# Kernel optimization log

Measured on AMD Instinct MI355X. Metric: run time of the kernel, lower is better.

The kernel has to match this reference:

```python
import jax, jax.numpy as jnp
import numpy as np

B, N, CQ, H, CH = 1, 256, 128, 4, 32  # batch, n_res, c_q(=c_k=c_v), heads, per-head dim


def setup_inputs() -> dict:
    key = jax.random.key(0)
    ks = jax.random.split(key, 12)
    s = 0.02
    q_x = jax.random.normal(ks[0], (B, N, N, CQ), jnp.float32)
    kv_x = jax.random.normal(ks[1], (B, N, N, CQ), jnp.float32)
    # mask bias: 0 where kept, -1e9 where masked (additive mask)
    keep = jax.random.uniform(ks[2], (B, N, 1, 1, N)) < 0.9
    mask_bias = jnp.where(keep, 0.0, -1e9).astype(jnp.float32)
    triangle_bias = jax.random.normal(ks[3], (B, 1, H, N, N), jnp.float32)
    # projection weights, stored per-head as [H, CH, C_in]
    wq = jax.random.normal(ks[4], (H, CH, CQ), jnp.float32) * s
    wk = jax.random.normal(ks[5], (H, CH, CQ), jnp.float32) * s
    wv = jax.random.normal(ks[6], (H, CH, CQ), jnp.float32) * s
    wg = jax.random.normal(ks[7], (H, CH, CQ), jnp.float32) * s
    bg = jax.random.normal(ks[8], (H, CH), jnp.float32) * s + 1.0  # gating bias init 1
    wo = jax.random.normal(ks[9], (CQ, H * CH), jnp.float32) * s
    bo = jnp.zeros((CQ,), jnp.float32)
    return {"q_x": q_x, "kv_x": kv_x, "mask_bias": mask_bias,
            "triangle_bias": triangle_bias, "wq": wq, "wk": wk, "wv": wv,
            "wg": wg, "bg": bg, "wo": wo, "bo": bo}


def reference(q_x, kv_x, mask_bias, triangle_bias, wq, wk, wv, wg, bg, wo, bo):
    scale = 1.0 / np.sqrt(CH).astype(np.float32)
    # project + split heads: [B,N,Q,C] x [H,D,C] -> [B,N,H,Q,D]
    q = jnp.einsum('bnqc,hdc->bnhqd', q_x, wq) * scale
    k = jnp.einsum('bnkc,hdc->bnhkd', kv_x, wk)
    v = jnp.einsum('bnkc,hdc->bnhkd', kv_x, wv)
    # scores + additive biases (mask_bias broadcasts over h,q; triangle over n)
    a = jnp.einsum('bnhqd,bnhkd->bnhqk', q, k) + mask_bias + triangle_bias
    a = jax.nn.softmax(a, axis=-1)
    o = jnp.einsum('bnhqk,bnhkd->bnhqd', a, v)
    o = jnp.swapaxes(o, -2, -3)  # [B,N,Q,H,D]
    # gating
    g = jax.nn.sigmoid(jnp.einsum('bnqc,hdc->bnqhd', q_x, wg) + bg)
    o = o * g
    o = o.reshape(o.shape[:-2] + (H * CH,))  # [B,N,Q,H*D]
    return jnp.einsum('bnqe,ce->bnqc', o, wo) + bo
```

## Files before the change

### kernel.cpp

```cpp
#include <hip/hip_runtime.h>

#define NRES 256
#define CIN  128
#define NH   4
#define DH   32

typedef __attribute__((ext_vector_type(4))) float f32x4;
typedef __attribute__((ext_vector_type(8))) short bf16x8;
typedef unsigned short u16;

#define U_WQG 0
#define U_WKV 32768
#define U_WWO 65536
#define U_QB  131072
#define U_KB  (U_QB + 8388608)
#define U_VT  (U_KB + 8388608)
#define U_GB  (U_VT + 8388608)
#define WS_NEED ((size_t)(U_GB + 8388608) * 2)

__device__ __forceinline__ unsigned pkbf(float a, float b) {
    unsigned ua = __builtin_bit_cast(unsigned, a);
    unsigned ub = __builtin_bit_cast(unsigned, b);
    ua += 0x7fffu + ((ua >> 16) & 1u);
    ub += 0x7fffu + ((ub >> 16) & 1u);
    return __builtin_amdgcn_perm(ub, ua, 0x07060302);
}
__device__ __forceinline__ u16 f2bfu(float f) {
    unsigned u = __builtin_bit_cast(unsigned, f);
    return (u16)((u + 0x7fffu + ((u >> 16) & 1u)) >> 16);
}
__device__ __forceinline__ float bf2f(u16 v) {
    unsigned u = ((unsigned)v) << 16;
    return __builtin_bit_cast(float, u);
}
union bfr { unsigned u[4]; bf16x8 v; };
__device__ __forceinline__ bf16x8 ldcvt8(const float* __restrict__ p) {
    f32x4 a = *(const f32x4*)p; f32x4 b = *(const f32x4*)(p + 4);
    bfr r;
    r.u[0] = pkbf(a[0], a[1]); r.u[1] = pkbf(a[2], a[3]);
    r.u[2] = pkbf(b[0], b[1]); r.u[3] = pkbf(b[2], b[3]);
    return r.v;
}
__device__ __forceinline__ bf16x8 ldcvt8s(const float* __restrict__ p, float sc) {
    f32x4 a = *(const f32x4*)p; f32x4 b = *(const f32x4*)(p + 4);
    bfr r;
    r.u[0] = pkbf(a[0] * sc, a[1] * sc); r.u[1] = pkbf(a[2] * sc, a[3] * sc);
    r.u[2] = pkbf(b[0] * sc, b[1] * sc); r.u[3] = pkbf(b[2] * sc, b[3] * sc);
    return r.v;
}
__device__ __forceinline__ void stage16(const float* __restrict__ p, u16* dst) {
    f32x4 a = *(const f32x4*)p,     b = *(const f32x4*)(p + 4);
    f32x4 c = *(const f32x4*)(p + 8), d = *(const f32x4*)(p + 12);
    bfr x, y;
    x.u[0] = pkbf(a[0], a[1]); x.u[1] = pkbf(a[2], a[3]);
    x.u[2] = pkbf(b[0], b[1]); x.u[3] = pkbf(b[2], b[3]);
    y.u[0] = pkbf(c[0], c[1]); y.u[1] = pkbf(c[2], c[3]);
    y.u[2] = pkbf(d[0], d[1]); y.u[3] = pkbf(d[2], d[3]);
    *(bf16x8*)dst = x.v;
    *(bf16x8*)(dst + 8) = y.v;
}
#define MFMA(a, b, c) __builtin_amdgcn_mfma_f32_16x16x32_bf16((a), (b), (c), 0, 0, 0)

__global__ void wconv(const float* __restrict__ wq, const float* __restrict__ wk,
                      const float* __restrict__ wv, const float* __restrict__ wg,
                      const float* __restrict__ wo, u16* __restrict__ ws)
{
    const int i0 = (blockIdx.x * 256 + threadIdx.x) * 8;
    const float qsc = 0.17677669529663687f;
    const float* src; u16* dst; float sc = 1.f;
    if (i0 < 32768) {
        const int e = i0 >> 7, c = i0 & 127;
        src = (e < 128 ? wq + e * CIN : wg + (e - 128) * CIN) + c;
        if (e < 128) sc = qsc;
        dst = ws + U_WQG + i0;
    } else if (i0 < 65536) {
        const int j = i0 - 32768, e = j >> 7, c = j & 127;
        src = (e < 128 ? wk + e * CIN : wv + (e - 128) * CIN) + c;
        dst = ws + U_WKV + j;
    } else {
        const int j = i0 - 65536;
        src = wo + j; dst = ws + U_WWO + j;
    }
    *(bf16x8*)dst = ldcvt8s(src, sc);
}

#define XST 136
__global__ __launch_bounds__(256, 4) void proj(
    const float* __restrict__ q_x, const float* __restrict__ kv_x,
    const float* __restrict__ bg, u16* __restrict__ ws)
{
    const int t = threadIdx.x, lane = t & 63, w = t >> 6;
    const int mrow = lane & 15, grp = lane >> 4;
    const int koff = grp * 8, rbase = grp * 4;
    const int R0 = blockIdx.x * 32;
    const int ysel = blockIdx.y;
    const float* __restrict__ src = ysel ? kv_x : q_x;
    const u16* __restrict__ W = ws + (ysel ? U_WKV : U_WQG);

    __shared__ u16 Xs[32 * XST];

    {
        const int row = t >> 3, c0 = (t & 7) * 16;
        stage16(src + (size_t)(R0 + row) * CIN + c0, &Xs[row * XST + c0]);
    }
    __syncthreads();

    const int cb = w * 64;
    const u16* __restrict__ Wc = W + (size_t)cb * CIN;

    const f32x4 zf = {0.f, 0.f, 0.f, 0.f};
    f32x4 acc[2][4];
    #pragma unroll
    for (int rt = 0; rt < 2; ++rt)
        #pragma unroll
        for (int nt = 0; nt < 4; ++nt) acc[rt][nt] = zf;

    #pragma unroll
    for (int ct = 0; ct < 4; ++ct) {
        const int c0 = ct * 32 + koff;
        bf16x8 a0 = *(const bf16x8*)&Xs[mrow * XST + c0];
        bf16x8 a1 = *(const bf16x8*)&Xs[(16 + mrow) * XST + c0];
        #pragma unroll
        for (int nt = 0; nt < 4; ++nt) {
            bf16x8 bw = *(const bf16x8*)(Wc + (size_t)(nt * 16 + mrow) * CIN + c0);
            acc[0][nt] = MFMA(a0, bw, acc[0][nt]);
            acc[1][nt] = MFMA(a1, bw, acc[1][nt]);
        }
    }

    if (!ysel) {
        if (cb < 128) {
            #pragma unroll
            for (int nt = 0; nt < 4; ++nt) {
                const int e = cb + nt * 16 + mrow;
                #pragma unroll
                for (int rt = 0; rt < 2; ++rt)
                    #pragma unroll
                    for (int r = 0; r < 4; ++r)
                        ws[U_QB + (size_t)(R0 + rt * 16 + rbase + r) * CIN + e] =
                            f2bfu(acc[rt][nt][r]);
            }
        } else {
            #pragma unroll
            for (int nt = 0; nt < 4; ++nt) {
                const int e = cb - 128 + nt * 16 + mrow;
                const float b = bg[e];
                #pragma unroll
                for (int rt = 0; rt < 2; ++rt)
                    #pragma unroll
                    for (int r = 0; r < 4; ++r) {
                        const float g = 1.f / (1.f + __expf(-(acc[rt][nt][r] + b)));
                        ws[U_GB + (size_t)(R0 + rt * 16 + rbase + r) * CIN + e] = f2bfu(g);
                    }
            }
        }
    } else {
        if (cb < 128) {
            #pragma unroll
            for (int nt = 0; nt < 4; ++nt) {
                const int e = cb + nt * 16 + mrow;
                #pragma unroll
                for (int rt = 0; rt < 2; ++rt)
                    #pragma unroll
                    for (int r = 0; r < 4; ++r)
                        ws[U_KB + (size_t)(R0 + rt * 16 + rbase + r) * CIN + e] =
                            f2bfu(acc[rt][nt][r]);
            }
        } else {
            const int n = R0 >> 8;
            #pragma unroll
            for (int nt = 0; nt < 4; ++nt) {
                const int d = cb - 128 + nt * 16 + mrow;
                #pragma unroll
                for (int rt = 0; rt < 2; ++rt) {
                    const int k0 = (R0 & 255) + rt * 16 + rbase;
                    uint2 v;
                    v.x = pkbf(acc[rt][nt][0], acc[rt][nt][1]);
                    v.y = pkbf(acc[rt][nt][2], acc[rt][nt][3]);
                    *(uint2*)&ws[U_VT + ((size_t)n * 128 + d) * 256 + k0] = v;
                }
            }
        }
    }
}

#define PST 40
__global__ __launch_bounds__(256, 4) void flash(
    const u16* __restrict__ ws, const float* __restrict__ mask_bias,
    const float* __restrict__ tri_bias, float* __restrict__ o_out)
{
    const int h = blockIdx.x, n = blockIdx.y;
    const int t = threadIdx.x, lane = t & 63, w = t >> 6;
    const int mrow = lane & 15, grp = lane >> 4;
    const int koff = grp * 8, rbase = grp * 4;
    const int q0 = w * 64;

    __shared__ u16 Pt[4 * 64 * PST];
    __shared__ float msk[NRES];

    if (t < 64) *(float4*)&msk[t * 4] = *(const float4*)(mask_bias + n * NRES + t * 4);

    const u16* __restrict__ Qb = ws + U_QB + (size_t)n * NRES * CIN;
    const u16* __restrict__ Kb = ws + U_KB + (size_t)n * NRES * CIN;
    const u16* __restrict__ Vt = ws + U_VT + (size_t)n * 128 * 256;
    const u16* __restrict__ Gb = ws + U_GB + (size_t)n * NRES * CIN;
    const float* __restrict__ trih = tri_bias + (size_t)h * NRES * NRES;

    bf16x8 bq[4];
    #pragma unroll
    for (int qt = 0; qt < 4; ++qt)
        bq[qt] = *(const bf16x8*)(Qb + (size_t)(q0 + qt * 16 + mrow) * CIN + h * DH + koff);
    __syncthreads();

    const f32x4 zf = {0.f, 0.f, 0.f, 0.f};
    f32x4 oa[4][2];
    float ls[4] = {0.f, 0.f, 0.f, 0.f};
    #pragma unroll
    for (int qt = 0; qt < 4; ++qt) { oa[qt][0] = zf; oa[qt][1] = zf; }

    u16* __restrict__ pw = &Pt[w * 64 * PST];

    for (int kt = 0; kt < 8; ++kt) {
        const int kb = kt * 32;
        bf16x8 ak0 = *(const bf16x8*)(Kb + (size_t)(kb + mrow) * CIN + h * DH + koff);
        bf16x8 ak1 = *(const bf16x8*)(Kb + (size_t)(kb + 16 + mrow) * CIN + h * DH + koff);
        bf16x8 bv0 = *(const bf16x8*)(Vt + (size_t)(h * DH + mrow) * NRES + kb + koff);
        bf16x8 bv1 = *(const bf16x8*)(Vt + (size_t)(h * DH + 16 + mrow) * NRES + kb + koff);
        f32x4 mk0 = *(const f32x4*)&msk[kb + rbase];
        f32x4 mk1 = *(const f32x4*)&msk[kb + 16 + rbase];
        #pragma unroll
        for (int r = 0; r < 4; ++r) { mk0[r] -= 8.f; mk1[r] -= 8.f; }

        #pragma unroll
        for (int qt = 0; qt < 4; ++qt) {
            f32x4 s0 = MFMA(ak0, bq[qt], zf);
            f32x4 s1 = MFMA(ak1, bq[qt], zf);
            const float* __restrict__ tq =
                trih + (size_t)(q0 + qt * 16 + mrow) * NRES + kb + rbase;
            f32x4 t0 = *(const f32x4*)tq;
            f32x4 t1 = *(const f32x4*)(tq + 16);
            #pragma unroll
            for (int r = 0; r < 4; ++r) {
                s0[r] = __expf(s0[r] + t0[r] + mk0[r]);
                s1[r] = __expf(s1[r] + t1[r] + mk1[r]);
            }
            ls[qt] += s0[0] + s0[1] + s0[2] + s0[3] + s1[0] + s1[1] + s1[2] + s1[3];
            uint2 p0, p1;
            p0.x = pkbf(s0[0], s0[1]); p0.y = pkbf(s0[2], s0[3]);
            p1.x = pkbf(s1[0], s1[1]); p1.y = pkbf(s1[2], s1[3]);
            *(uint2*)&pw[(qt * 16 + mrow) * PST + rbase] = p0;
            *(uint2*)&pw[(qt * 16 + mrow) * PST + 16 + rbase] = p1;
        }
        asm volatile("s_waitcnt lgkmcnt(0)" ::: "memory");
        #pragma unroll
        for (int qt = 0; qt < 4; ++qt) {
            bf16x8 pa = *(const bf16x8*)&pw[(qt * 16 + mrow) * PST + koff];
            oa[qt][0] = MFMA(pa, bv0, oa[qt][0]);
            oa[qt][1] = MFMA(pa, bv1, oa[qt][1]);
        }
    }

    float* __restrict__ orow = o_out + (size_t)n * NRES * CIN + h * DH;
    #pragma unroll
    for (int qt = 0; qt < 4; ++qt) {
        float lred = ls[qt];
        lred += __shfl_xor(lred, 16, 64);
        lred += __shfl_xor(lred, 32, 64);
        const float linv = 1.f / lred;
        #pragma unroll
        for (int r = 0; r < 4; ++r) {
            const float iv = __shfl(linv, rbase + r, 64);
            const int q = q0 + qt * 16 + rbase + r;
            const float g0 = bf2f(Gb[(size_t)q * CIN + h * DH + mrow]);
            const float g1 = bf2f(Gb[(size_t)q * CIN + h * DH + 16 + mrow]);
            orow[q * CIN + mrow]      = oa[qt][0][r] * iv * g0;
            orow[q * CIN + 16 + mrow] = oa[qt][1][r] * iv * g1;
        }
    }
}

__global__ __launch_bounds__(256, 4) void gout(
    const u16* __restrict__ ws, const float* __restrict__ bo, float* io)
{
    const int t = threadIdx.x, lane = t & 63, w = t >> 6;
    const int mrow = lane & 15, grp = lane >> 4;
    const int koff = grp * 8, rbase = grp * 4;
    const int r0 = blockIdx.x * 64;
    const u16* __restrict__ Wo = ws + U_WWO;

    __shared__ u16 Xs[64 * XST];

    {
        const int row = t >> 2, c0 = (t & 3) * 32;
        const float* p = io + (size_t)(r0 + row) * CIN + c0;
        stage16(p,      &Xs[row * XST + c0]);
        stage16(p + 16, &Xs[row * XST + c0 + 16]);
    }
    __syncthreads();

    const int rw = w * 16;
    const f32x4 zf = {0.f, 0.f, 0.f, 0.f};
    f32x4 acc[8];
    #pragma unroll
    for (int nt = 0; nt < 8; ++nt) acc[nt] = zf;

    #pragma unroll
    for (int ct = 0; ct < 4; ++ct) {
        const int c0 = ct * 32 + koff;
        bf16x8 a0 = *(const bf16x8*)&Xs[(rw + mrow) * XST + c0];
        #pragma unroll
        for (int nt = 0; nt < 8; ++nt) {
            bf16x8 bw = *(const bf16x8*)(Wo + (size_t)(nt * 16 + mrow) * CIN + c0);
            acc[nt] = MFMA(a0, bw, acc[nt]);
        }
    }

    #pragma unroll
    for (int nt = 0; nt < 8; ++nt) {
        const float bc = bo[nt * 16 + mrow];
        #pragma unroll
        for (int r = 0; r < 4; ++r)
            io[(size_t)(r0 + rw + rbase + r) * CIN + nt * 16 + mrow] = acc[nt][r] + bc;
    }
}

#define KST 32
#define VST 264
#define GST 136

__global__ __launch_bounds__(256, 3) void attn_fb(
    const float* __restrict__ q_x, const float* __restrict__ kv_x,
    const float* __restrict__ mask_bias, const float* __restrict__ tri_bias,
    const float* __restrict__ wq, const float* __restrict__ wk,
    const float* __restrict__ wv, float* __restrict__ o_out)
{
    const int h = blockIdx.x, n = blockIdx.y;
    const int t = threadIdx.x;
    const int lane = t & 63, w = t >> 6;
    const int mrow = lane & 15;
    const int grp  = lane >> 4;
    const int koff = grp * 8;
    const int rbase = grp * 4;
    const int q0 = w * 64;

    __shared__ u16 Ks[NRES * KST];
    __shared__ u16 Vt[DH * VST];
    __shared__ u16 Ptb[4 * 32 * PST];
    __shared__ float msk[NRES];

    if (t < 64) *(float4*)&msk[t * 4] = *(const float4*)(mask_bias + n * NRES + t * 4);

    const float* __restrict__ qxn = q_x  + (size_t)n * NRES * CIN;
    const float* __restrict__ kxn = kv_x + (size_t)n * NRES * CIN;
    const float* __restrict__ wqh = wq + h * DH * CIN;
    const float* __restrict__ wkh = wk + h * DH * CIN;
    const float* __restrict__ wvh = wv + h * DH * CIN;

    f32x4 aq_[4][2], ak_[4][2], av_[4][2];
    const f32x4 zf = {0.f, 0.f, 0.f, 0.f};
    #pragma unroll
    for (int qt = 0; qt < 4; ++qt)
        #pragma unroll
        for (int dt = 0; dt < 2; ++dt) { aq_[qt][dt] = zf; ak_[qt][dt] = zf; av_[qt][dt] = zf; }

    const float qsc = 0.17677669529663687f;
    #pragma unroll
    for (int ct = 0; ct < 4; ++ct) {
        const int c0 = ct * 32 + koff;
        bf16x8 bq0 = ldcvt8s(wqh + mrow * CIN + c0, qsc);
        bf16x8 bq1 = ldcvt8s(wqh + (16 + mrow) * CIN + c0, qsc);
        bf16x8 bk0 = ldcvt8(wkh + mrow * CIN + c0);
        bf16x8 bk1 = ldcvt8(wkh + (16 + mrow) * CIN + c0);
        bf16x8 bv0 = ldcvt8(wvh + mrow * CIN + c0);
        bf16x8 bv1 = ldcvt8(wvh + (16 + mrow) * CIN + c0);
        #pragma unroll
        for (int qt = 0; qt < 4; ++qt) {
            bf16x8 aX = ldcvt8(qxn + (q0 + qt * 16 + mrow) * CIN + c0);
            aq_[qt][0] = MFMA(aX, bq0, aq_[qt][0]);
            aq_[qt][1] = MFMA(aX, bq1, aq_[qt][1]);
            bf16x8 aK = ldcvt8(kxn + (q0 + qt * 16 + mrow) * CIN + c0);
            ak_[qt][0] = MFMA(aK, bk0, ak_[qt][0]);
            ak_[qt][1] = MFMA(aK, bk1, ak_[qt][1]);
            av_[qt][0] = MFMA(aK, bv0, av_[qt][0]);
            av_[qt][1] = MFMA(aK, bv1, av_[qt][1]);
        }
    }

    #pragma unroll
    for (int qt = 0; qt < 4; ++qt)
        #pragma unroll
        for (int dt = 0; dt < 2; ++dt)
            #pragma unroll
            for (int r = 0; r < 4; ++r) {
                const int row = q0 + qt * 16 + rbase + r;
                const int d = dt * 16 + mrow;
                Ks[row * KST + d] = f2bfu(ak_[qt][dt][r]);
                Vt[d * VST + row] = f2bfu(av_[qt][dt][r]);
            }

    u16* __restrict__ pw = &Ptb[w * 32 * PST];
    bf16x8 aq[4];
    #pragma unroll
    for (int h2 = 0; h2 < 2; ++h2) {
        #pragma unroll
        for (int j = 0; j < 2; ++j) {
            const int qt = h2 * 2 + j;
            #pragma unroll
            for (int dt = 0; dt < 2; ++dt)
                #pragma unroll
                for (int r = 0; r < 4; ++r)
                    pw[(j * 16 + rbase + r) * PST + dt * 16 + mrow] = f2bfu(aq_[qt][dt][r]);
        }
        asm volatile("s_waitcnt lgkmcnt(0)" ::: "memory");
        #pragma unroll
        for (int j = 0; j < 2; ++j)
            aq[h2 * 2 + j] = *(const bf16x8*)&pw[(j * 16 + mrow) * PST + koff];
        asm volatile("s_waitcnt lgkmcnt(0)" ::: "memory");
    }
    __syncthreads();

    f32x4 oa[4][2], ls4[4];
    #pragma unroll
    for (int qt = 0; qt < 4; ++qt) { oa[qt][0] = zf; oa[qt][1] = zf; ls4[qt] = zf; }

    const float* __restrict__ trih = tri_bias + (size_t)h * NRES * NRES;

    for (int kt = 0; kt < 8; ++kt) {
        const int kb = kt * 32;
        bf16x8 bk0 = *(const bf16x8*)&Ks[(kb + mrow) * KST + koff];
        bf16x8 bk1 = *(const bf16x8*)&Ks[(kb + 16 + mrow) * KST + koff];
        bf16x8 bv0 = *(const bf16x8*)&Vt[mrow * VST + kb + koff];
        bf16x8 bv1 = *(const bf16x8*)&Vt[(16 + mrow) * VST + kb + koff];
        const float mb0 = msk[kb + mrow] - 8.f;
        const float mb1 = msk[kb + 16 + mrow] - 8.f;

        #pragma unroll
        for (int h2 = 0; h2 < 2; ++h2) {
            float tr0[2][4], tr1[2][4];
            #pragma unroll
            for (int j = 0; j < 2; ++j) {
                const int qt = h2 * 2 + j;
                const float* __restrict__ trow =
                    trih + (q0 + qt * 16 + rbase) * NRES + kb + mrow;
                #pragma unroll
                for (int r = 0; r < 4; ++r) {
                    tr0[j][r] = trow[r * NRES];
                    tr1[j][r] = trow[r * NRES + 16];
                }
            }
            #pragma unroll
            for (int j = 0; j < 2; ++j) {
                const int qt = h2 * 2 + j;
                f32x4 s0 = MFMA(aq[qt], bk0, zf);
                f32x4 s1 = MFMA(aq[qt], bk1, zf);
                #pragma unroll
                for (int r = 0; r < 4; ++r) {
                    s0[r] = __expf(s0[r] + tr0[j][r] + mb0);
                    s1[r] = __expf(s1[r] + tr1[j][r] + mb1);
                }
                ls4[qt] += s0 + s1;
                #pragma unroll
                for (int r = 0; r < 4; ++r) {
                    pw[(j * 16 + rbase + r) * PST + mrow]      = f2bfu(s0[r]);
                    pw[(j * 16 + rbase + r) * PST + 16 + mrow] = f2bfu(s1[r]);
                }
            }
            asm volatile("s_waitcnt lgkmcnt(0)" ::: "memory");
            #pragma unroll
            for (int j = 0; j < 2; ++j) {
                const int qt = h2 * 2 + j;
                bf16x8 pa = *(const bf16x8*)&pw[(j * 16 + mrow) * PST + koff];
                oa[qt][0] = MFMA(pa, bv0, oa[qt][0]);
                oa[qt][1] = MFMA(pa, bv1, oa[qt][1]);
            }
        }
    }

    float* __restrict__ orow = o_out + (size_t)n * NRES * CIN + h * DH;
    #pragma unroll
    for (int qt = 0; qt < 4; ++qt) {
        f32x4 lv = ls4[qt];
        #pragma unroll
        for (int xm = 1; xm < 16; xm <<= 1) {
            lv[0] += __shfl_xor(lv[0], xm, 64);
            lv[1] += __shfl_xor(lv[1], xm, 64);
            lv[2] += __shfl_xor(lv[2], xm, 64);
            lv[3] += __shfl_xor(lv[3], xm, 64);
        }
        #pragma unroll
        for (int r = 0; r < 4; ++r) {
            const float inv = 1.f / lv[r];
            const int q = q0 + qt * 16 + rbase + r;
            orow[q * CIN + mrow]      = oa[qt][0][r] * inv;
            orow[q * CIN + 16 + mrow] = oa[qt][1][r] * inv;
        }
    }
}

__global__ __launch_bounds__(256, 4) void gate_fb(
    const float* __restrict__ q_x, const float* __restrict__ wg,
    const float* __restrict__ bg, const float* __restrict__ wo,
    const float* __restrict__ bo, float* io)
{
    const int t = threadIdx.x;
    const int lane = t & 63, w = t >> 6;
    const int mrow = lane & 15, grp = lane >> 4;
    const int koff = grp * 8, rbase = grp * 4;
    const int r0 = blockIdx.x * 128 + w * 32;

    __shared__ u16 Gt[4 * 32 * GST];
    u16* __restrict__ gw = &Gt[w * 32 * GST];

    const f32x4 zf = {0.f, 0.f, 0.f, 0.f};
    f32x4 acc[2][8];
    #pragma unroll
    for (int at = 0; at < 2; ++at)
        #pragma unroll
        for (int nt = 0; nt < 8; ++nt) acc[at][nt] = zf;

    #pragma unroll
    for (int ks = 0; ks < 4; ++ks) {
        const int c0 = ks * 32 + koff;
        bf16x8 ax0 = ldcvt8(q_x + (size_t)(r0 + mrow) * CIN + c0);
        bf16x8 ax1 = ldcvt8(q_x + (size_t)(r0 + 16 + mrow) * CIN + c0);
        #pragma unroll
        for (int nt = 0; nt < 8; ++nt) {
            bf16x8 bw = ldcvt8(wg + (nt * 16 + mrow) * CIN + c0);
            acc[0][nt] = MFMA(ax0, bw, acc[0][nt]);
            acc[1][nt] = MFMA(ax1, bw, acc[1][nt]);
        }
    }

    #pragma unroll
    for (int nt = 0; nt < 8; ++nt) {
        const float bge = bg[nt * 16 + mrow];
        #pragma unroll
        for (int at = 0; at < 2; ++at)
            #pragma unroll
            for (int r = 0; r < 4; ++r) {
                const int qg = r0 + at * 16 + rbase + r;
                const float ov = io[(size_t)qg * CIN + nt * 16 + mrow];
                const float g = 1.f / (1.f + __expf(-(acc[at][nt][r] + bge)));
                gw[(at * 16 + rbase + r) * GST + nt * 16 + mrow] = f2bfu(ov * g);
            }
    }
    asm volatile("s_waitcnt lgkmcnt(0)" ::: "memory");

    f32x4 acc2[2][8];
    #pragma unroll
    for (int at = 0; at < 2; ++at)
        #pragma unroll
        for (int nt = 0; nt < 8; ++nt) acc2[at][nt] = zf;

    #pragma unroll
    for (int ks = 0; ks < 4; ++ks) {
        const int e0 = ks * 32 + koff;
        bf16x8 ag0 = *(const bf16x8*)&gw[mrow * GST + e0];
        bf16x8 ag1 = *(const bf16x8*)&gw[(16 + mrow) * GST + e0];
        #pragma unroll
        for (int nt = 0; nt < 8; ++nt) {
            bf16x8 bw = ldcvt8(wo + (nt * 16 + mrow) * CIN + e0);
            acc2[0][nt] = MFMA(ag0, bw, acc2[0][nt]);
            acc2[1][nt] = MFMA(ag1, bw, acc2[1][nt]);
        }
    }

    #pragma unroll
    for (int nt = 0; nt < 8; ++nt) {
        const float boc = bo[nt * 16 + mrow];
        #pragma unroll
        for (int at = 0; at < 2; ++at)
            #pragma unroll
            for (int r = 0; r < 4; ++r)
                io[(size_t)(r0 + at * 16 + rbase + r) * CIN + nt * 16 + mrow] =
                    acc2[at][nt][r] + boc;
    }
}

extern "C" void kernel_launch(void* const* d_in, const int* in_sizes, int n_in,
                              void* d_out, int out_size, void* d_ws, size_t ws_size,
                              hipStream_t stream) {
    const float* q_x  = (const float*)d_in[0];
    const float* kv_x = (const float*)d_in[1];
    const float* mask = (const float*)d_in[2];
    const float* tri  = (const float*)d_in[3];
    const float* wq   = (const float*)d_in[4];
    const float* wk   = (const float*)d_in[5];
    const float* wv   = (const float*)d_in[6];
    const float* wg   = (const float*)d_in[7];
    const float* bg   = (const float*)d_in[8];
    const float* wo   = (const float*)d_in[9];
    const float* bo   = (const float*)d_in[10];
    float* out = (float*)d_out;

    if (ws_size >= WS_NEED) {
        u16* ws16 = (u16*)d_ws;
        wconv<<<40, 256, 0, stream>>>(wq, wk, wv, wg, wo, ws16);
        proj<<<dim3(2048, 2), 256, 0, stream>>>(q_x, kv_x, bg, ws16);
        flash<<<dim3(NH, NRES), 256, 0, stream>>>(ws16, mask, tri, out);
        gout<<<1024, 256, 0, stream>>>(ws16, bo, out);
    } else {
        attn_fb<<<dim3(NH, NRES), 256, 0, stream>>>(q_x, kv_x, mask, tri, wq, wk, wv, out);
        gate_fb<<<(NRES * NRES) / 128, 256, 0, stream>>>(q_x, wg, bg, wo, bo, out);
    }
}
```

Before: 246.4 us.

## Fuse output projection into flash attention kernel, looping heads per block

Merges the flash attention and the output projection (gout) kernels. Each block now owns 64 query rows, and each wave handles 16 rows across all four heads in a loop. The gated per-head output is rounded to bf16 in LDS and multiplied straight into Wo, accumulating the final output in registers. This removes the fp32 intermediate write, the re-read and one kernel launch. In exchange, each wave re-reads K/V for every head with less query reuse per K/V load, there is less parallelism inside each head, and the per-iteration LDS waits are serialized.

```diff
diff --git a/kernel.cpp b/kernel.cpp
--- a/kernel.cpp
+++ b/kernel.cpp
@@ -185,17 +185,18 @@
 }
 
 #define PST 40
-__global__ __launch_bounds__(256, 4) void flash(
+__global__ __launch_bounds__(256, 4) void flashout(
     const u16* __restrict__ ws, const float* __restrict__ mask_bias,
-    const float* __restrict__ tri_bias, float* __restrict__ o_out)
+    const float* __restrict__ tri_bias, const float* __restrict__ bo,
+    float* __restrict__ out)
 {
-    const int h = blockIdx.x, n = blockIdx.y;
+    const int n = blockIdx.y;
     const int t = threadIdx.x, lane = t & 63, w = t >> 6;
     const int mrow = lane & 15, grp = lane >> 4;
     const int koff = grp * 8, rbase = grp * 4;
-    const int q0 = w * 64;
-
-    __shared__ u16 Pt[4 * 64 * PST];
+    const int q0 = blockIdx.x * 64 + w * 16;
+
+    __shared__ u16 Pt[4 * 16 * PST];
     __shared__ float msk[NRES];
 
     if (t < 64) *(float4*)&msk[t * 4] = *(const float4*)(mask_bias + n * NRES + t * 4);
@@ -204,123 +205,87 @@
     const u16* __restrict__ Kb = ws + U_KB + (size_t)n * NRES * CIN;
     const u16* __restrict__ Vt = ws + U_VT + (size_t)n * 128 * 256;
     const u16* __restrict__ Gb = ws + U_GB + (size_t)n * NRES * CIN;
-    const float* __restrict__ trih = tri_bias + (size_t)h * NRES * NRES;
-
-    bf16x8 bq[4];
-    #pragma unroll
-    for (int qt = 0; qt < 4; ++qt)
-        bq[qt] = *(const bf16x8*)(Qb + (size_t)(q0 + qt * 16 + mrow) * CIN + h * DH + koff);
+    const u16* __restrict__ Wo = ws + U_WWO;
+
+    u16* __restrict__ pw = &Pt[w * 16 * PST];
     __syncthreads();
 
     const f32x4 zf = {0.f, 0.f, 0.f, 0.f};
-    f32x4 oa[4][2];
-    float ls[4] = {0.f, 0.f, 0.f, 0.f};
-    #pragma unroll
-    for (int qt = 0; qt < 4; ++qt) { oa[qt][0] = zf; oa[qt][1] = zf; }
-
-    u16* __restrict__ pw = &Pt[w * 64 * PST];
-
-    for (int kt = 0; kt < 8; ++kt) {
-        const int kb = kt * 32;
-        bf16x8 ak0 = *(const bf16x8*)(Kb + (size_t)(kb + mrow) * CIN + h * DH + koff);
-        bf16x8 ak1 = *(const bf16x8*)(Kb + (size_t)(kb + 16 + mrow) * CIN + h * DH + koff);
-        bf16x8 bv0 = *(const bf16x8*)(Vt + (size_t)(h * DH + mrow) * NRES + kb + koff);
-        bf16x8 bv1 = *(const bf16x8*)(Vt + (size_t)(h * DH + 16 + mrow) * NRES + kb + koff);
-        f32x4 mk0 = *(const f32x4*)&msk[kb + rbase];
-        f32x4 mk1 = *(const f32x4*)&msk[kb + 16 + rbase];
-        #pragma unroll
-        for (int r = 0; r < 4; ++r) { mk0[r] -= 8.f; mk1[r] -= 8.f; }
-
-        #pragma unroll
-        for (int qt = 0; qt < 4; ++qt) {
-            f32x4 s0 = MFMA(ak0, bq[qt], zf);
-            f32x4 s1 = MFMA(ak1, bq[qt], zf);
+    f32x4 oacc[8];
+    #pragma unroll
+    for (int nt = 0; nt < 8; ++nt) oacc[nt] = zf;
+
+    for (int h = 0; h < NH; ++h) {
+        const int e0 = h * DH + koff;
+        const float* __restrict__ trih = tri_bias + (size_t)h * NRES * NRES;
+
+        bf16x8 bq = *(const bf16x8*)(Qb + (size_t)(q0 + mrow) * CIN + e0);
+
+        f32x4 ov0 = zf, ov1 = zf;
+        float ls = 0.f;
+
+        for (int kt = 0; kt < 8; ++kt) {
+            const int kb = kt * 32;
+            bf16x8 ak0 = *(const bf16x8*)(Kb + (size_t)(kb + mrow) * CIN + e0);
+            bf16x8 ak1 = *(const bf16x8*)(Kb + (size_t)(kb + 16 + mrow) * CIN + e0);
+            bf16x8 bv0 = *(const bf16x8*)(Vt + (size_t)(h * DH + mrow) * NRES + kb + koff);
+            bf16x8 bv1 = *(const bf16x8*)(Vt + (size_t)(h * DH + 16 + mrow) * NRES + kb + koff);
+            f32x4 mk0 = *(const f32x4*)&msk[kb + rbase];
+            f32x4 mk1 = *(const f32x4*)&msk[kb + 16 + rbase];
+
+            f32x4 s0 = MFMA(ak0, bq, zf);
+            f32x4 s1 = MFMA(ak1, bq, zf);
             const float* __restrict__ tq =
-                trih + (size_t)(q0 + qt * 16 + mrow) * NRES + kb + rbase;
+                trih + (size_t)(q0 + mrow) * NRES + kb + rbase;
             f32x4 t0 = *(const f32x4*)tq;
             f32x4 t1 = *(const f32x4*)(tq + 16);
             #pragma unroll
             for (int r = 0; r < 4; ++r) {
-                s0[r] = __expf(s0[r] + t0[r] + mk0[r]);
-                s1[r] = __expf(s1[r] + t1[r] + mk1[r]);
-            }
-            ls[qt] += s0[0] + s0[1] + s0[2] + s0[3] + s1[0] + s1[1] + s1[2] + s1[3];
+                s0[r] = __expf(s0[r] + t0[r] + mk0[r] - 8.f);
+                s1[r] = __expf(s1[r] + t1[r] + mk1[r] - 8.f);
+            }
+            ls += s0[0] + s0[1] + s0[2] + s0[3] + s1[0] + s1[1] + s1[2] + s1[3];
             uint2 p0, p1;
             p0.x = pkbf(s0[0], s0[1]); p0.y = pkbf(s0[2], s0[3]);
             p1.x = pkbf(s1[0], s1[1]); p1.y = pkbf(s1[2], s1[3]);
-            *(uint2*)&pw[(qt * 16 + mrow) * PST + rbase] = p0;
-            *(uint2*)&pw[(qt * 16 + mrow) * PST + 16 + rbase] = p1;
-        }
-        asm volatile("s_waitcnt lgkmcnt(0)" ::: "memory");
-        #pragma unroll
-        for (int qt = 0; qt < 4; ++qt) {
-            bf16x8 pa = *(const bf16x8*)&pw[(qt * 16 + mrow) * PST + koff];
-            oa[qt][0] = MFMA(pa, bv0, oa[qt][0]);
-            oa[qt][1] = MFMA(pa, bv1, oa[qt][1]);
-        }
-    }
-
-    float* __restrict__ orow = o_out + (size_t)n * NRES * CIN + h * DH;
-    #pragma unroll
-    for (int qt = 0; qt < 4; ++qt) {
-        float lred = ls[qt];
-        lred += __shfl_xor(lred, 16, 64);
-        lred += __shfl_xor(lred, 32, 64);
-        const float linv = 1.f / lred;
+            *(uint2*)&pw[mrow * PST + rbase] = p0;
+            *(uint2*)&pw[mrow * PST + 16 + rbase] = p1;
+            asm volatile("s_waitcnt lgkmcnt(0)" ::: "memory");
+            bf16x8 pa = *(const bf16x8*)&pw[mrow * PST + koff];
+            ov0 = MFMA(pa, bv0, ov0);
+            ov1 = MFMA(pa, bv1, ov1);
+        }
+
+        ls += __shfl_xor(ls, 16, 64);
+        ls += __shfl_xor(ls, 32, 64);
+        const float linv = 1.f / ls;
+
         #pragma unroll
         for (int r = 0; r < 4; ++r) {
             const float iv = __shfl(linv, rbase + r, 64);
-            const int q = q0 + qt * 16 + rbase + r;
+            const int q = q0 + rbase + r;
             const float g0 = bf2f(Gb[(size_t)q * CIN + h * DH + mrow]);
             const float g1 = bf2f(Gb[(size_t)q * CIN + h * DH + 16 + mrow]);
-            orow[q * CIN + mrow]      = oa[qt][0][r] * iv * g0;
-            orow[q * CIN + 16 + mrow] = oa[qt][1][r] * iv * g1;
-        }
-    }
-}
-
-__global__ __launch_bounds__(256, 4) void gout(
-    const u16* __restrict__ ws, const float* __restrict__ bo, float* io)
-{
-    const int t = threadIdx.x, lane = t & 63, w = t >> 6;
-    const int mrow = lane & 15, grp = lane >> 4;
-    const int koff = grp * 8, rbase = grp * 4;
-    const int r0 = blockIdx.x * 64;
-    const u16* __restrict__ Wo = ws + U_WWO;
-
-    __shared__ u16 Xs[64 * XST];
-
-    {
-        const int row = t >> 2, c0 = (t & 3) * 32;
-        const float* p = io + (size_t)(r0 + row) * CIN + c0;
-        stage16(p,      &Xs[row * XST + c0]);
-        stage16(p + 16, &Xs[row * XST + c0 + 16]);
-    }
-    __syncthreads();
-
-    const int rw = w * 16;
-    const f32x4 zf = {0.f, 0.f, 0.f, 0.f};
-    f32x4 acc[8];
-    #pragma unroll
-    for (int nt = 0; nt < 8; ++nt) acc[nt] = zf;
-
-    #pragma unroll
-    for (int ct = 0; ct < 4; ++ct) {
-        const int c0 = ct * 32 + koff;
-        bf16x8 a0 = *(const bf16x8*)&Xs[(rw + mrow) * XST + c0];
+            pw[(rbase + r) * PST + mrow]      = f2bfu(ov0[r] * iv * g0);
+            pw[(rbase + r) * PST + 16 + mrow] = f2bfu(ov1[r] * iv * g1);
+        }
+        asm volatile("s_waitcnt lgkmcnt(0)" ::: "memory");
+        bf16x8 og = *(const bf16x8*)&pw[mrow * PST + koff];
+
         #pragma unroll
         for (int nt = 0; nt < 8; ++nt) {
-            bf16x8 bw = *(const bf16x8*)(Wo + (size_t)(nt * 16 + mrow) * CIN + c0);
-            acc[nt] = MFMA(a0, bw, acc[nt]);
-        }
-    }
-
+            bf16x8 bwo = *(const bf16x8*)(Wo + (size_t)(nt * 16 + mrow) * CIN + e0);
+            oacc[nt] = MFMA(og, bwo, oacc[nt]);
+        }
+    }
+
+    float* __restrict__ orow = out + ((size_t)n * NRES + q0) * CIN;
     #pragma unroll
     for (int nt = 0; nt < 8; ++nt) {
         const float bc = bo[nt * 16 + mrow];
         #pragma unroll
         for (int r = 0; r < 4; ++r)
-            io[(size_t)(r0 + rw + rbase + r) * CIN + nt * 16 + mrow] = acc[nt][r] + bc;
+            orow[(rbase + r) * CIN + nt * 16 + mrow] = oacc[nt][r] + bc;
     }
 }
 
@@ -597,8 +562,7 @@
         u16* ws16 = (u16*)d_ws;
         wconv<<<40, 256, 0, stream>>>(wq, wk, wv, wg, wo, ws16);
         proj<<<dim3(2048, 2), 256, 0, stream>>>(q_x, kv_x, bg, ws16);
-        flash<<<dim3(NH, NRES), 256, 0, stream>>>(ws16, mask, tri, out);
-        gout<<<1024, 256, 0, stream>>>(ws16, bo, out);
+        flashout<<<dim3(4, NRES), 256, 0, stream>>>(ws16, mask, tri, bo, out);
     } else {
         attn_fb<<<dim3(NH, NRES), 256, 0, stream>>>(q_x, kv_x, mask, tri, wq, wk, wv, out);
         gate_fb<<<(NRES * NRES) / 128, 256, 0, stream>>>(q_x, wg, bg, wo, bo, out);
```

After: 268.4 us. 1.09x slower.
